# Kernel tuning notes

Hardware: AMD Instinct MI355X
Metric: run time of the kernel (lower is better)

The kernel has to match this reference:

```python
import jax, jax.numpy as jnp
import numpy as np


def setup_inputs() -> dict:
    key = jax.random.key(0)
    ks = jax.random.split(key, 7)
    B, T, I, H, O = 64, 1024, 256, 512, 256
    s_i = 1.0 / np.sqrt(I)
    s_h = 1.0 / np.sqrt(H)
    return {
        "x": jax.random.normal(ks[0], (B, T, I), dtype=jnp.float32),
        "Wi": jax.random.normal(ks[1], (H, I), dtype=jnp.float32) * s_i,
        "bi": jax.random.normal(ks[2], (H,), dtype=jnp.float32) * s_i,
        "Wh": jax.random.normal(ks[3], (H, H), dtype=jnp.float32) * s_h,
        "bh": jax.random.normal(ks[4], (H,), dtype=jnp.float32) * s_h,
        "Wo": jax.random.normal(ks[5], (O, H), dtype=jnp.float32) * s_h,
        "bo": jax.random.normal(ks[6], (O,), dtype=jnp.float32) * s_h,
    }


def reference(x, Wi, bi, Wh, bh, Wo, bo):
    # x: [B, T, I]; recurrent tanh RNN, return final linear projection [B, O]
    B, T, I = x.shape
    H = Wi.shape[0]
    # Precompute input projections for all steps at once: [T, B, H]
    xproj = jnp.einsum('bti,hi->tbh', x, Wi) + bi + bh

    def step(h, xp_t):
        h_next = jnp.tanh(xp_t + h @ Wh.T)
        return h_next, None

    h0 = jnp.zeros((B, H), dtype=x.dtype)
    h_final, _ = jax.lax.scan(step, h0, xproj)
    return h_final @ Wo.T + bo
```

## Files before the change

### kernel.cpp

```cpp
#include <hip/hip_runtime.h>
#include <math.h>

#define Bsz 64
#define Tlen 1024
#define Idim 256
#define Hdim 512
#define Odim 256

#define PB  2
#define NSL 8
#define NG  (Bsz / PB)
#define FLAG_STRIDE 64

__global__ __launch_bounds__(256) void xproj_kernel(
        const float* __restrict__ x, const float* __restrict__ Wi,
        const float* __restrict__ bi, const float* __restrict__ bh,
        float* __restrict__ xp, int t0, int CT) {
    __shared__ float As[16][132];
    __shared__ float Bs[16][132];
    const int tid = threadIdx.x;
    const int bm = blockIdx.x, bn = blockIdx.y;
    const int tx = tid & 15, ty = tid >> 4;

    const int f0 = tid, f1 = tid + 256;
    const int ar0 = f0 >> 2, ak0 = (f0 & 3) * 4;
    const int ar1 = f1 >> 2, ak1 = (f1 & 3) * 4;
    const int m0g = bm * 128 + ar0;
    const int m1g = bm * 128 + ar1;
    const int b0 = m0g / CT, tt0 = m0g - b0 * CT;
    const int b1 = m1g / CT, tt1 = m1g - b1 * CT;
    const float* xrow0 = x + ((size_t)b0 * Tlen + t0 + tt0) * Idim;
    const float* xrow1 = x + ((size_t)b1 * Tlen + t0 + tt1) * Idim;
    const float* wrow0 = Wi + (size_t)(bn * 128 + ar0) * Idim;
    const float* wrow1 = Wi + (size_t)(bn * 128 + ar1) * Idim;

    float acc[8][8];
#pragma unroll
    for (int i = 0; i < 8; ++i)
#pragma unroll
        for (int j = 0; j < 8; ++j) acc[i][j] = 0.0f;

    for (int kk = 0; kk < Idim; kk += 16) {
        float4 av0 = *(const float4*)(xrow0 + kk + ak0);
        float4 av1 = *(const float4*)(xrow1 + kk + ak1);
        float4 bv0 = *(const float4*)(wrow0 + kk + ak0);
        float4 bv1 = *(const float4*)(wrow1 + kk + ak1);
        __syncthreads();
        As[ak0 + 0][ar0] = av0.x; As[ak0 + 1][ar0] = av0.y;
        As[ak0 + 2][ar0] = av0.z; As[ak0 + 3][ar0] = av0.w;
        As[ak1 + 0][ar1] = av1.x; As[ak1 + 1][ar1] = av1.y;
        As[ak1 + 2][ar1] = av1.z; As[ak1 + 3][ar1] = av1.w;
        Bs[ak0 + 0][ar0] = bv0.x; Bs[ak0 + 1][ar0] = bv0.y;
        Bs[ak0 + 2][ar0] = bv0.z; Bs[ak0 + 3][ar0] = bv0.w;
        Bs[ak1 + 0][ar1] = bv1.x; Bs[ak1 + 1][ar1] = bv1.y;
        Bs[ak1 + 2][ar1] = bv1.z; Bs[ak1 + 3][ar1] = bv1.w;
        __syncthreads();
#pragma unroll
        for (int k = 0; k < 16; ++k) {
            float4 a0 = *(const float4*)&As[k][tx * 4];
            float4 a1 = *(const float4*)&As[k][64 + tx * 4];
            float4 bq0 = *(const float4*)&Bs[k][ty * 4];
            float4 bq1 = *(const float4*)&Bs[k][64 + ty * 4];
            float a[8] = {a0.x, a0.y, a0.z, a0.w, a1.x, a1.y, a1.z, a1.w};
            float bb[8] = {bq0.x, bq0.y, bq0.z, bq0.w, bq1.x, bq1.y, bq1.z, bq1.w};
#pragma unroll
            for (int i = 0; i < 8; ++i)
#pragma unroll
                for (int j = 0; j < 8; ++j) acc[i][j] += a[i] * bb[j];
        }
    }

    const int n0 = bn * 128;
    float biasv[8];
#pragma unroll
    for (int j = 0; j < 8; ++j) {
        int c = (j < 4) ? (ty * 4 + j) : (64 + ty * 4 + (j - 4));
        biasv[j] = bi[n0 + c] + bh[n0 + c];
    }
#pragma unroll
    for (int i = 0; i < 8; ++i) {
        int r = (i < 4) ? (tx * 4 + i) : (64 + tx * 4 + (i - 4));
        size_t mrow = (size_t)(bm * 128 + r);
        float4 o0 = {acc[i][0] + biasv[0], acc[i][1] + biasv[1],
                     acc[i][2] + biasv[2], acc[i][3] + biasv[3]};
        float4 o1 = {acc[i][4] + biasv[4], acc[i][5] + biasv[5],
                     acc[i][6] + biasv[6], acc[i][7] + biasv[7]};
        *(float4*)(xp + mrow * Hdim + n0 + ty * 4) = o0;
        *(float4*)(xp + mrow * Hdim + n0 + 64 + ty * 4) = o1;
    }
}

__global__ void init_flags(int* flags) {
    int i = blockIdx.x * blockDim.x + threadIdx.x;
    if (i < NG * FLAG_STRIDE) flags[i] = 0;
}

__global__ __launch_bounds__(512) void scan_reg(
        const float* __restrict__ xp, const float* __restrict__ Wh,
        float* __restrict__ hglob, int* __restrict__ flags, int t0, int CT) {
    const int wg = blockIdx.x;
    const int g = (wg & 7) + ((wg >> 6) << 3);
    const int n = (wg >> 3) & 7;
    const int colbase = n * 64;
    const int bbase = g * PB;
    const int tid = threadIdx.x;
    const int ct = tid & 15;
    const int kg = tid >> 4;

    float4 w[4][4];
#pragma unroll
    for (int cc = 0; cc < 4; ++cc) {
        const float4* src =
            (const float4*)(Wh + (size_t)(colbase + ct * 4 + cc) * Hdim + kg * 16);
#pragma unroll
        for (int i = 0; i < 4; ++i) w[cc][i] = src[i];
    }

    __shared__ float  hs[PB][Hdim];
    __shared__ float4 red4[PB][32][17];

    if (tid < 256) {
        const int b = tid >> 7, q = tid & 127;
        const size_t base = ((size_t)(t0 & 1) * Bsz + bbase + b) * Hdim + q * 4;
#pragma unroll
        for (int j = 0; j < 4; ++j) {
            float v = 0.f;
            if (t0 != 0)
                v = __hip_atomic_load(&hglob[base + j], __ATOMIC_RELAXED,
                                      __HIP_MEMORY_SCOPE_AGENT);
            hs[b][q * 4 + j] = v;
        }
    }
    __syncthreads();

    const int fb = tid >> 6;
    const int fc = tid & 63;
    int* const flag = &flags[g * FLAG_STRIDE];

    float xv = 0.f;
    if (tid < 128)
        xv = xp[((size_t)(bbase + fb) * CT) * Hdim + colbase + fc];

    for (int t = 0; t < CT; ++t) {
        const int st = t0 + t;
        const int nb = (st + 1) & 1;

        float4 p0 = {0.f, 0.f, 0.f, 0.f};
        float4 p1 = {0.f, 0.f, 0.f, 0.f};
#pragma unroll
        for (int i = 0; i < 4; ++i) {
            float4 h0 = *(const float4*)&hs[0][kg * 16 + i * 4];
            float4 h1 = *(const float4*)&hs[1][kg * 16 + i * 4];
            p0.x += w[0][i].x * h0.x + w[0][i].y * h0.y + w[0][i].z * h0.z + w[0][i].w * h0.w;
            p0.y += w[1][i].x * h0.x + w[1][i].y * h0.y + w[1][i].z * h0.z + w[1][i].w * h0.w;
            p0.z += w[2][i].x * h0.x + w[2][i].y * h0.y + w[2][i].z * h0.z + w[2][i].w * h0.w;
            p0.w += w[3][i].x * h0.x + w[3][i].y * h0.y + w[3][i].z * h0.z + w[3][i].w * h0.w;
            p1.x += w[0][i].x * h1.x + w[0][i].y * h1.y + w[0][i].z * h1.z + w[0][i].w * h1.w;
            p1.y += w[1][i].x * h1.x + w[1][i].y * h1.y + w[1][i].z * h1.z + w[1][i].w * h1.w;
            p1.z += w[2][i].x * h1.x + w[2][i].y * h1.y + w[2][i].z * h1.z + w[2][i].w * h1.w;
            p1.w += w[3][i].x * h1.x + w[3][i].y * h1.y + w[3][i].z * h1.z + w[3][i].w * h1.w;
        }
        red4[0][kg][ct] = p0;
        red4[1][kg][ct] = p1;
        __syncthreads();

        if (tid < 128) {
            float s = 0.f;
#pragma unroll
            for (int k = 0; k < 32; ++k)
                s += ((const float*)&red4[fb][k][0])[fc];
            float h1v = tanhf(s + xv);
            __hip_atomic_store(
                &hglob[((size_t)nb * Bsz + bbase + fb) * Hdim + colbase + fc],
                h1v, __ATOMIC_RELAXED, __HIP_MEMORY_SCOPE_AGENT);
            hs[fb][colbase + fc] = h1v;
        }
        __syncthreads();

        if (tid == 0)
            __hip_atomic_fetch_add(flag, 1, __ATOMIC_RELAXED,
                                   __HIP_MEMORY_SCOPE_AGENT);

        if (tid < 128 && t + 1 < CT)
            xv = xp[((size_t)(bbase + fb) * CT + (t + 1)) * Hdim + colbase + fc];

        if (tid == 0) {
            while (__hip_atomic_load(flag, __ATOMIC_RELAXED,
                                     __HIP_MEMORY_SCOPE_AGENT) < NSL * (st + 1)) {}
        }
        __syncthreads();

        if (tid < 256) {
            const int b = tid >> 7, q = tid & 127;
            if ((q >> 4) != n) {
                const size_t base =
                    ((size_t)nb * Bsz + bbase + b) * Hdim + q * 4;
#pragma unroll
                for (int j = 0; j < 4; ++j)
                    hs[b][q * 4 + j] =
                        __hip_atomic_load(&hglob[base + j], __ATOMIC_RELAXED,
                                          __HIP_MEMORY_SCOPE_AGENT);
            }
        }
        __syncthreads();
    }
}

__global__ __launch_bounds__(256) void out_kernel(
        const float* __restrict__ hbuf, const float* __restrict__ Wo,
        const float* __restrict__ bo, float* __restrict__ out) {
    __shared__ float hsh[Hdim];
    const int b = blockIdx.x, o = threadIdx.x;
    hsh[o] = hbuf[b * Hdim + o];
    hsh[o + 256] = hbuf[b * Hdim + o + 256];
    __syncthreads();
    const float4* wrow = (const float4*)(Wo + (size_t)o * Hdim);
    const float4* h4 = (const float4*)hsh;
    float4 a4 = {0.0f, 0.0f, 0.0f, 0.0f};
#pragma unroll 4
    for (int i = 0; i < Hdim / 4; ++i) {
        float4 ww = wrow[i];
        float4 hv = h4[i];
        a4.x += ww.x * hv.x;
        a4.y += ww.y * hv.y;
        a4.z += ww.z * hv.z;
        a4.w += ww.w * hv.w;
    }
    out[b * Odim + o] = bo[o] + ((a4.x + a4.y) + (a4.z + a4.w));
}

extern "C" void kernel_launch(void* const* d_in, const int* in_sizes, int n_in,
                              void* d_out, int out_size, void* d_ws, size_t ws_size,
                              hipStream_t stream) {
    const float* x  = (const float*)d_in[0];
    const float* Wi = (const float*)d_in[1];
    const float* bi = (const float*)d_in[2];
    const float* Wh = (const float*)d_in[3];
    const float* bh = (const float*)d_in[4];
    const float* Wo = (const float*)d_in[5];
    const float* bo = (const float*)d_in[6];
    float* out = (float*)d_out;

    const size_t hbytes = 2ull * Bsz * Hdim * sizeof(float);
    const size_t fbytes = (size_t)NG * FLAG_STRIDE * sizeof(int);
    const size_t extrabytes = hbytes + fbytes;
    int CT = Tlen;
    while (CT > 2 && (size_t)Bsz * CT * Hdim * sizeof(float) + extrabytes > ws_size)
        CT >>= 1;

    float* xp    = (float*)d_ws;
    float* hglob = (float*)((char*)d_ws + (size_t)Bsz * CT * Hdim * sizeof(float));
    int*   flags = (int*)((char*)hglob + hbytes);

    init_flags<<<dim3((NG * FLAG_STRIDE + 255) / 256), 256, 0, stream>>>(flags);
    for (int t0 = 0; t0 < Tlen; t0 += CT) {
        xproj_kernel<<<dim3((Bsz * CT) / 128, Hdim / 128), 256, 0, stream>>>(
            x, Wi, bi, bh, xp, t0, CT);
        scan_reg<<<dim3(NG * NSL), 512, 0, stream>>>(xp, Wh, hglob, flags, t0, CT);
    }
    out_kernel<<<dim3(Bsz), 256, 0, stream>>>(hglob, Wo, bo, out);
}
```

Before: 2.450 ms.

## Replace flag-counter barrier with step-tagged 64-bit hidden-state polling

Each hidden-state element is now stored as a 64-bit word that packs the float value with the step number it belongs to. Consumer threads spin directly on the foreign elements they need until the expected tag appears. This removes the per-group atomic counter, the single-thread spin, one block-wide barrier per step and the flag init kernel, so blocks depend only on the data they read. The costs are doubled hidden-state traffic from the 64-bit words, many threads polling global memory at once, and an x-projection prefetch moved earlier in the step.

```diff
diff --git a/kernel.cpp b/kernel.cpp
--- a/kernel.cpp
+++ b/kernel.cpp
@@ -1,5 +1,7 @@
 #include <hip/hip_runtime.h>
 #include <math.h>
+
+typedef unsigned long long ulong_t;
 
 #define Bsz 64
 #define Tlen 1024
@@ -10,7 +12,6 @@
 #define PB  2
 #define NSL 8
 #define NG  (Bsz / PB)
-#define FLAG_STRIDE 64
 
 __global__ __launch_bounds__(256) void xproj_kernel(
         const float* __restrict__ x, const float* __restrict__ Wi,
@@ -90,14 +91,9 @@
     }
 }
 
-__global__ void init_flags(int* flags) {
-    int i = blockIdx.x * blockDim.x + threadIdx.x;
-    if (i < NG * FLAG_STRIDE) flags[i] = 0;
-}
-
 __global__ __launch_bounds__(512) void scan_reg(
         const float* __restrict__ xp, const float* __restrict__ Wh,
-        float* __restrict__ hglob, int* __restrict__ flags, int t0, int CT) {
+        ulong_t* __restrict__ hglob, int t0, int CT) {
     const int wg = blockIdx.x;
     const int g = (wg & 7) + ((wg >> 6) << 3);
     const int n = (wg >> 3) & 7;
@@ -119,23 +115,25 @@
     __shared__ float  hs[PB][Hdim];
     __shared__ float4 red4[PB][32][17];
 
-    if (tid < 256) {
-        const int b = tid >> 7, q = tid & 127;
-        const size_t base = ((size_t)(t0 & 1) * Bsz + bbase + b) * Hdim + q * 4;
-#pragma unroll
-        for (int j = 0; j < 4; ++j) {
-            float v = 0.f;
-            if (t0 != 0)
-                v = __hip_atomic_load(&hglob[base + j], __ATOMIC_RELAXED,
-                                      __HIP_MEMORY_SCOPE_AGENT);
-            hs[b][q * 4 + j] = v;
-        }
+    const int pb_ = tid >> 8;
+    const int pc  = (tid & 255) * 2;
+    const bool foreign = ((pc >> 6) != n);
+
+    {
+        float v0 = 0.f, v1 = 0.f;
+        if (t0 != 0) {
+            const ulong_t* a =
+                hglob + (((size_t)(t0 & 1)) * Bsz + bbase + pb_) * Hdim + pc;
+            v0 = __uint_as_float((unsigned)a[0]);
+            v1 = __uint_as_float((unsigned)a[1]);
+        }
+        hs[pb_][pc] = v0;
+        hs[pb_][pc + 1] = v1;
     }
     __syncthreads();
 
     const int fb = tid >> 6;
     const int fc = tid & 63;
-    int* const flag = &flags[g * FLAG_STRIDE];
 
     float xv = 0.f;
     if (tid < 128)
@@ -164,55 +162,59 @@
         red4[1][kg][ct] = p1;
         __syncthreads();
 
+        float xv_next = 0.f;
+        if (tid < 128 && t + 1 < CT)
+            xv_next = xp[((size_t)(bbase + fb) * CT + (t + 1)) * Hdim + colbase + fc];
+
         if (tid < 128) {
             float s = 0.f;
 #pragma unroll
             for (int k = 0; k < 32; ++k)
                 s += ((const float*)&red4[fb][k][0])[fc];
             float h1v = tanhf(s + xv);
+            ulong_t pk = (((ulong_t)(unsigned)(st + 1)) << 32) |
+                         (ulong_t)__float_as_uint(h1v);
             __hip_atomic_store(
                 &hglob[((size_t)nb * Bsz + bbase + fb) * Hdim + colbase + fc],
-                h1v, __ATOMIC_RELAXED, __HIP_MEMORY_SCOPE_AGENT);
+                pk, __ATOMIC_RELAXED, __HIP_MEMORY_SCOPE_AGENT);
             hs[fb][colbase + fc] = h1v;
         }
-        __syncthreads();
-
-        if (tid == 0)
-            __hip_atomic_fetch_add(flag, 1, __ATOMIC_RELAXED,
-                                   __HIP_MEMORY_SCOPE_AGENT);
-
-        if (tid < 128 && t + 1 < CT)
-            xv = xp[((size_t)(bbase + fb) * CT + (t + 1)) * Hdim + colbase + fc];
-
-        if (tid == 0) {
-            while (__hip_atomic_load(flag, __ATOMIC_RELAXED,
-                                     __HIP_MEMORY_SCOPE_AGENT) < NSL * (st + 1)) {}
-        }
-        __syncthreads();
-
-        if (tid < 256) {
-            const int b = tid >> 7, q = tid & 127;
-            if ((q >> 4) != n) {
-                const size_t base =
-                    ((size_t)nb * Bsz + bbase + b) * Hdim + q * 4;
-#pragma unroll
-                for (int j = 0; j < 4; ++j)
-                    hs[b][q * 4 + j] =
-                        __hip_atomic_load(&hglob[base + j], __ATOMIC_RELAXED,
-                                          __HIP_MEMORY_SCOPE_AGENT);
+        xv = xv_next;
+
+        if (t + 1 < CT) {
+            if (foreign) {
+                ulong_t* a =
+                    hglob + ((size_t)nb * Bsz + bbase + pb_) * Hdim + pc;
+                const unsigned tagexp = (unsigned)(st + 1);
+                ulong_t x0 = 0, x1 = 0;
+                bool d0 = false, d1 = false;
+                do {
+                    if (!d0) {
+                        x0 = __hip_atomic_load(a, __ATOMIC_RELAXED,
+                                               __HIP_MEMORY_SCOPE_AGENT);
+                        d0 = ((unsigned)(x0 >> 32) == tagexp);
+                    }
+                    if (!d1) {
+                        x1 = __hip_atomic_load(a + 1, __ATOMIC_RELAXED,
+                                               __HIP_MEMORY_SCOPE_AGENT);
+                        d1 = ((unsigned)(x1 >> 32) == tagexp);
+                    }
+                } while (!(d0 && d1));
+                hs[pb_][pc]     = __uint_as_float((unsigned)x0);
+                hs[pb_][pc + 1] = __uint_as_float((unsigned)x1);
             }
-        }
-        __syncthreads();
+            __syncthreads();
+        }
     }
 }
 
 __global__ __launch_bounds__(256) void out_kernel(
-        const float* __restrict__ hbuf, const float* __restrict__ Wo,
+        const ulong_t* __restrict__ hbuf, const float* __restrict__ Wo,
         const float* __restrict__ bo, float* __restrict__ out) {
     __shared__ float hsh[Hdim];
     const int b = blockIdx.x, o = threadIdx.x;
-    hsh[o] = hbuf[b * Hdim + o];
-    hsh[o + 256] = hbuf[b * Hdim + o + 256];
+    hsh[o]       = __uint_as_float((unsigned)hbuf[(size_t)b * Hdim + o]);
+    hsh[o + 256] = __uint_as_float((unsigned)hbuf[(size_t)b * Hdim + o + 256]);
     __syncthreads();
     const float4* wrow = (const float4*)(Wo + (size_t)o * Hdim);
     const float4* h4 = (const float4*)hsh;
@@ -241,22 +243,18 @@
     const float* bo = (const float*)d_in[6];
     float* out = (float*)d_out;
 
-    const size_t hbytes = 2ull * Bsz * Hdim * sizeof(float);
-    const size_t fbytes = (size_t)NG * FLAG_STRIDE * sizeof(int);
-    const size_t extrabytes = hbytes + fbytes;
+    const size_t hbytes = 2ull * Bsz * Hdim * sizeof(ulong_t);
     int CT = Tlen;
-    while (CT > 2 && (size_t)Bsz * CT * Hdim * sizeof(float) + extrabytes > ws_size)
+    while (CT > 2 && (size_t)Bsz * CT * Hdim * sizeof(float) + hbytes > ws_size)
         CT >>= 1;
 
-    float* xp    = (float*)d_ws;
-    float* hglob = (float*)((char*)d_ws + (size_t)Bsz * CT * Hdim * sizeof(float));
-    int*   flags = (int*)((char*)hglob + hbytes);
-
-    init_flags<<<dim3((NG * FLAG_STRIDE + 255) / 256), 256, 0, stream>>>(flags);
+    float*   xp    = (float*)d_ws;
+    ulong_t* hglob = (ulong_t*)((char*)d_ws + (size_t)Bsz * CT * Hdim * sizeof(float));
+
     for (int t0 = 0; t0 < Tlen; t0 += CT) {
         xproj_kernel<<<dim3((Bsz * CT) / 128, Hdim / 128), 256, 0, stream>>>(
             x, Wi, bi, bh, xp, t0, CT);
-        scan_reg<<<dim3(NG * NSL), 512, 0, stream>>>(xp, Wh, hglob, flags, t0, CT);
+        scan_reg<<<dim3(NG * NSL), 512, 0, stream>>>(xp, Wh, hglob, t0, CT);
     }
     out_kernel<<<dim3(Bsz), 256, 0, stream>>>(hglob, Wo, bo, out);
 }
```

After: 2.559 ms. 1.04x slower.
